# Performance work log

Measured on AMD Instinct MI355X. Metric: run time of the kernel, lower is better.

Reference implementation:

```python
import jax, jax.numpy as jnp
import numpy as np

NUM_CODES = 1024
CODE_DIM = 256
COMMIT_W = 0.25
EPS = 1e-5
ENT_LO, ENT_HI = 0.5, 0.9
ENT_W = 0.1
VAR_FLOOR = 0.05
VAR_W = 1e-3
DECORR_W = 1e-3


def setup_inputs() -> dict:
    key = jax.random.key(0)
    k1, k2, k3 = jax.random.split(key, 3)
    inputs = jax.random.normal(k1, (16, 2048, CODE_DIM), dtype=jnp.float32)
    weight = jax.random.normal(k2, (NUM_CODES, CODE_DIM), dtype=jnp.float32) * 0.1
    usage_counts = jax.random.uniform(k3, (NUM_CODES,), dtype=jnp.float32)
    return {"inputs": inputs, "weight": weight, "usage_counts": usage_counts}


def reference(inputs, weight, usage_counts):
    K, D = weight.shape
    flat = inputs.reshape(-1, D)  # [N, D]
    # squared euclidean distances [N, K]
    dist = (flat ** 2).sum(axis=1, keepdims=True) - 2.0 * flat @ weight.T + (weight ** 2).sum(axis=1)
    idx = jnp.argmin(dist, axis=1)  # [N]
    quant = weight[idx].reshape(inputs.shape)

    commitment_loss = COMMIT_W * jnp.mean((jax.lax.stop_gradient(quant) - inputs) ** 2)
    # straight-through estimator
    quant_ste = inputs + jax.lax.stop_gradient(quant - inputs)

    # usage entropy regularizer
    probs = usage_counts + EPS
    probs = probs / jnp.maximum(probs.sum(), EPS * K)
    usage_entropy = -jnp.sum(probs * jnp.log(probs + EPS)) / np.log(float(K)).astype(np.float32)
    gap = jnp.where(usage_entropy < ENT_LO, ENT_LO - usage_entropy,
                    jnp.where(usage_entropy > ENT_HI, usage_entropy - ENT_HI, 0.0))
    entropy_loss = ENT_W * gap ** 2

    # variance floor penalty on codebook
    variance = jnp.var(weight, axis=0)
    variance_loss = VAR_W * jnp.mean(jax.nn.relu(VAR_FLOOR - variance))

    # decorrelation penalty
    wc = weight - weight.mean(axis=0, keepdims=True)
    cov = wc.T @ wc / float(K)  # [D, D]
    off_diag = cov - jnp.diag(jnp.diag(cov))
    decorrelation_loss = DECORR_W * jnp.mean(off_diag ** 2)

    total_loss = commitment_loss + entropy_loss + variance_loss + decorrelation_loss
    indices = idx.reshape(inputs.shape[:-1])
    return (quant_ste, indices, total_loss, commitment_loss, entropy_loss,
            variance_loss, decorrelation_loss, usage_entropy)
```

## Files before the change

kernel.cpp:

```cpp
#include <hip/hip_runtime.h>
#include <math.h>

#define DIMS   256
#define KCODES 1024
#define NTOT   32768
#define TAU    4.0e-4f

typedef __bf16 bf16x8 __attribute__((ext_vector_type(8)));
typedef float  f32x4  __attribute__((ext_vector_type(4)));

#define WS_COMMIT   0
#define WS_FLAGCNT  1
#define WS_DECORR   2
#define WS_COLSUM   16
#define WS_COLSQ    272
#define WS_WSQ      1024
#define WS_XSQ      2048
#define WS_FLAGS    34816
#define WS_CAND1    67584
#define WS_CAND2    329728
#define WS_CANDI    591872
#define WS_WP       854016

#define OUT_Q    0
#define OUT_IDX  8388608
#define OUT_SCAL 8421376


__global__ __launch_bounds__(256) void prep_kernel(const float* __restrict__ X,
                                                   const float* __restrict__ W,
                                                   __bf16* __restrict__ Xp,
                                                   __bf16* __restrict__ Wp2,
                                                   float* ws) {
  int b = blockIdx.x;
  int tid = threadIdx.x;
  if (b < 1056) {
    bool isW = b >= 1024;
    const float* src = isW ? W : X;
    __bf16* dst = isW ? Wp2 : Xp;
    int sqoff = isW ? WS_WSQ : WS_XSQ;
    int bb = isW ? b - 1024 : b;
    int kt = tid >> 5, mtl = (tid >> 4) & 1, lc = tid & 15;
    int row = bb * 32 + mtl * 16 + lc;
    int bt = row >> 7, c = row & 127;
    int wv = c >> 6, t = (c >> 4) & 3;
    size_t hibase = ((((size_t)(bt * 8 + kt) * 2 + wv) * 4 + t) * 2) * 512;
    const float* s = src + (size_t)row * DIMS + kt * 32;
    float sq = 0.f;
    #pragma unroll
    for (int kq = 0; kq < 4; kq++) {
      float4 u = *(const float4*)(s + kq * 8);
      float4 v = *(const float4*)(s + kq * 8 + 4);
      float f[8] = {u.x, u.y, u.z, u.w, v.x, v.y, v.z, v.w};
      bf16x8 hi, lo;
      #pragma unroll
      for (int e = 0; e < 8; e++) {
        __bf16 h = (__bf16)f[e];
        hi[e] = h;
        lo[e] = (__bf16)(f[e] - (float)h);
        sq = fmaf(f[e], f[e], sq);
      }
      size_t off = (size_t)(kq * 16 + lc) * 8;
      *(bf16x8*)&dst[hibase + off] = hi;
      *(bf16x8*)&dst[hibase + 512 + off] = lo;
    }
    atomicAdd(&ws[sqoff + row], sq);
  } else if (b < 1064) {
    int d = tid;
    int r0 = (b - 1056) * 128;
    float s = 0.f, sq = 0.f;
    #pragma unroll 8
    for (int k = 0; k < 128; k++) {
      float v = W[(size_t)(r0 + k) * DIMS + d];
      s += v;
      sq = fmaf(v, v, sq);
    }
    atomicAdd(&ws[WS_COLSUM + d], s);
    atomicAdd(&ws[WS_COLSQ + d], sq);
  } else {
    __shared__ float wi_s[KCODES];
    __shared__ float red2[256];
    __shared__ float miB;
    __shared__ float red[4];
    int i0 = b - 1064;
    #pragma unroll
    for (int q = 0; q < 4; q++) {
      int row = q * 256 + tid;
      wi_s[row] = W[(size_t)row * DIMS + i0];
    }
    __syncthreads();
    float pm = 0.f;
    #pragma unroll
    for (int q = 0; q < 4; q++) pm += wi_s[tid * 4 + q];
    red2[tid] = pm;
    __syncthreads();
    if (tid == 0) {
      float s = 0.f;
      for (int k = 0; k < 256; k++) s += red2[k];
      miB = s * (1.0f / 1024.0f);
    }
    int j = tid;
    float a0 = 0.f, sj = 0.f;
    for (int k = 0; k < KCODES; k += 4) {
      #pragma unroll
      for (int u = 0; u < 4; u++) {
        float wj = W[(size_t)(k + u) * DIMS + j];
        a0 = fmaf(wi_s[k + u], wj, a0);
        sj += wj;
      }
    }
    __syncthreads();
    const float inv = 1.0f / 1024.0f;
    float mj = sj * inv;
    float v = 0.f;
    float c0 = a0 * inv - miB * mj;
    if (i0 != j) v = c0 * c0;
    #pragma unroll
    for (int m = 32; m >= 1; m >>= 1) v += __shfl_xor(v, m);
    if ((j & 63) == 0) red[j >> 6] = v;
    __syncthreads();
    if (j == 0) atomicAdd(&ws[WS_DECORR], (red[0] + red[1]) + (red[2] + red[3]));
  }
}

__global__ __launch_bounds__(256, 2) void pass1_kernel(const __bf16* __restrict__ Xp,
                                                       const __bf16* __restrict__ Wp2,
                                                       float* ws) {
  __shared__ float wsqs[128];
  __shared__ float d1L[256];
  __shared__ float d2L[256];
  __shared__ int   i1L[256];

  int tid = threadIdx.x;
  int lane = tid & 63, wave = tid >> 6;
  int wm = wave >> 1, wn = wave & 1;
  int quad = lane >> 4, col = lane & 15;
  int l = blockIdx.x;
  int bm = (l & 7) * 32 + ((l >> 3) & 31);
  int bn = l >> 8;
  int rowBase = bm * 128, cb = bn * 128;

  if (tid < 128) wsqs[tid] = ws[WS_WSQ + cb + tid];

  f32x4 acc[4][4];
  #pragma unroll
  for (int i = 0; i < 4; i++)
    #pragma unroll
    for (int j = 0; j < 4; j++) acc[i][j] = (f32x4){0.f, 0.f, 0.f, 0.f};

  const bf16x8* ab = (const bf16x8*)(Xp + (size_t)bm * 65536 + wm * 4096) + lane;
  const bf16x8* bb = (const bf16x8*)(Wp2 + (size_t)bn * 65536 + wn * 4096) + lane;

  bf16x8 Af[2][8], Bf[2][8];
  #pragma unroll
  for (int f = 0; f < 4; f++) {
    Af[0][f * 2] = ab[f * 128];
    Af[0][f * 2 + 1] = ab[f * 128 + 64];
    Bf[0][f * 2] = bb[f * 128];
    Bf[0][f * 2 + 1] = bb[f * 128 + 64];
  }
  #pragma unroll
  for (int kt = 0; kt < 8; kt++) {
    const int cur = kt & 1, nxt = cur ^ 1;
    if (kt < 7) {
      const bf16x8* an = ab + (kt + 1) * 1024;
      const bf16x8* bv = bb + (kt + 1) * 1024;
      #pragma unroll
      for (int f = 0; f < 4; f++) {
        Af[nxt][f * 2] = an[f * 128];
        Af[nxt][f * 2 + 1] = an[f * 128 + 64];
        Bf[nxt][f * 2] = bv[f * 128];
        Bf[nxt][f * 2 + 1] = bv[f * 128 + 64];
      }
    }
    #pragma unroll
    for (int nt = 0; nt < 4; nt++) {
      #pragma unroll
      for (int mt = 0; mt < 4; mt++) {
        acc[mt][nt] = __builtin_amdgcn_mfma_f32_16x16x32_bf16(Af[cur][mt * 2], Bf[cur][nt * 2], acc[mt][nt], 0, 0, 0);
        acc[mt][nt] = __builtin_amdgcn_mfma_f32_16x16x32_bf16(Af[cur][mt * 2], Bf[cur][nt * 2 + 1], acc[mt][nt], 0, 0, 0);
        acc[mt][nt] = __builtin_amdgcn_mfma_f32_16x16x32_bf16(Af[cur][mt * 2 + 1], Bf[cur][nt * 2], acc[mt][nt], 0, 0, 0);
      }
    }
  }
  __syncthreads();

  #pragma unroll
  for (int mt = 0; mt < 4; mt++) {
    #pragma unroll
    for (int r = 0; r < 4; r++) {
      float d1 = 3.0e38f, d2 = 3.0e38f;
      int i1 = 0;
      #pragma unroll
      for (int nt = 0; nt < 4; nt++) {
        int lc = wn * 64 + nt * 16 + col;
        float d = wsqs[lc] - 2.0f * acc[mt][nt][r];
        int g = cb + lc;
        if (d < d1) { d2 = d1; d1 = d; i1 = g; }
        else if (d < d2) d2 = d;
      }
      #pragma unroll
      for (int m = 1; m < 16; m <<= 1) {
        float od1 = __shfl_xor(d1, m);
        int oi1 = __shfl_xor(i1, m);
        float od2 = __shfl_xor(d2, m);
        if (od1 < d1 || (od1 == d1 && oi1 < i1)) {
          d2 = fminf(d1, fminf(d2, od2));
          d1 = od1; i1 = oi1;
        } else {
          d2 = fminf(od1, fminf(d2, od2));
        }
      }
      if (col == 0) {
        int lr = wm * 64 + mt * 16 + quad * 4 + r;
        d1L[lr * 2 + wn] = d1;
        d2L[lr * 2 + wn] = d2;
        i1L[lr * 2 + wn] = i1;
      }
    }
  }
  __syncthreads();
  if (tid < 128) {
    float a1 = d1L[tid * 2], a2 = d2L[tid * 2];
    int ai = i1L[tid * 2];
    float b1 = d1L[tid * 2 + 1], b2 = d2L[tid * 2 + 1];
    int bi = i1L[tid * 2 + 1];
    float m1, m2; int mi;
    if (b1 < a1 || (b1 == a1 && bi < ai)) { m1 = b1; mi = bi; m2 = fminf(a1, b2); }
    else { m1 = a1; mi = ai; m2 = fminf(b1, a2); }
    int o = bn * NTOT + rowBase + tid;
    ws[WS_CAND1 + o] = m1;
    ws[WS_CAND2 + o] = m2;
    ((int*)ws)[WS_CANDI + o] = mi;
  }
}

__global__ __launch_bounds__(256) void pass2_kernel(const float* __restrict__ W,
                                                    float* __restrict__ outQ,
                                                    float* __restrict__ outIdx, float* ws) {
  __shared__ float p1L[4][64];
  __shared__ float p2L[4][64];
  __shared__ int   piL[4][64];
  __shared__ int   idx_s[64];
  int tid = threadIdx.x;
  int r0 = blockIdx.x * 64;
  int grp = tid >> 6, rl = tid & 63;
  int row = r0 + rl;
  const float* c1 = ws + WS_CAND1;
  const float* c2 = ws + WS_CAND2;
  const int* ci = (const int*)ws + WS_CANDI;
  {
    int oa = (2 * grp) * NTOT + row;
    int ob = (2 * grp + 1) * NTOT + row;
    float a1 = c1[oa], a2 = c2[oa];
    int ai = ci[oa];
    float b1 = c1[ob], b2 = c2[ob];
    int bi = ci[ob];
    float m1, m2; int mi;
    if (b1 < a1 || (b1 == a1 && bi < ai)) { m1 = b1; mi = bi; m2 = fminf(a1, b2); }
    else { m1 = a1; mi = ai; m2 = fminf(a2, b1); }
    p1L[grp][rl] = m1;
    p2L[grp][rl] = m2;
    piL[grp][rl] = mi;
  }
  __syncthreads();
  if (tid < 64) {
    float m1 = p1L[0][tid], m2 = p2L[0][tid];
    int mi = piL[0][tid];
    #pragma unroll
    for (int w = 1; w < 4; w++) {
      float b1 = p1L[w][tid], b2 = p2L[w][tid];
      int bi = piL[w][tid];
      if (b1 < m1 || (b1 == m1 && bi < mi)) { m2 = fminf(m1, b2); m1 = b1; mi = bi; }
      else { m2 = fminf(m2, b1); }
    }
    int rw = r0 + tid;
    outIdx[rw] = (float)mi;
    idx_s[tid] = mi;
    int* wsI = (int*)ws;
    if (m2 - m1 < TAU) {
      int p = atomicAdd(&wsI[WS_FLAGCNT], 1);
      wsI[WS_FLAGS + p] = rw;
    }
    float partial = ws[WS_XSQ + rw] + m1;
    #pragma unroll
    for (int m = 32; m >= 1; m >>= 1) partial += __shfl_xor(partial, m);
    if (tid == 0) atomicAdd(&ws[WS_COMMIT], partial);
  }
  __syncthreads();
  int wave = tid >> 6, lane = tid & 63;
  #pragma unroll 4
  for (int i = 0; i < 16; i++) {
    int rr = wave * 16 + i;
    int ix = idx_s[rr];
    float4 v = ((const float4*)(W + (size_t)ix * DIMS))[lane];
    ((float4*)(outQ + (size_t)(r0 + rr) * DIMS))[lane] = v;
  }
}

__global__ __launch_bounds__(256) void refine_kernel(const float* __restrict__ X,
                                                     const float* __restrict__ W,
                                                     float* __restrict__ outQ,
                                                     float* __restrict__ outIdx, float* ws,
                                                     const float* __restrict__ U,
                                                     float* __restrict__ out) {
  __shared__ float xs[DIMS];
  __shared__ double dm[256];
  __shared__ int im[256];
  __shared__ int chosen;
  int tid = threadIdx.x;
  if (blockIdx.x == 512) {
    __shared__ float red[256];
    float s = 0.f;
    for (int e = tid; e < KCODES; e += 256) s += U[e] + 1e-5f;
    red[tid] = s;
    __syncthreads();
    for (int st = 128; st >= 1; st >>= 1) {
      if (tid < st) red[tid] += red[tid + st];
      __syncthreads();
    }
    float S = red[0];
    __syncthreads();
    float denom = fmaxf(S, 1e-5f * 1024.0f);
    float h = 0.f;
    for (int e = tid; e < KCODES; e += 256) {
      float p = (U[e] + 1e-5f) / denom;
      h += p * logf(p + 1e-5f);
    }
    red[tid] = h;
    __syncthreads();
    for (int st = 128; st >= 1; st >>= 1) {
      if (tid < st) red[tid] += red[tid + st];
      __syncthreads();
    }
    float H = -red[0] / 6.93147180559945f;
    __syncthreads();
    float m = ws[WS_COLSUM + tid] * (1.0f / 1024.0f);
    float var = ws[WS_COLSQ + tid] * (1.0f / 1024.0f) - m * m;
    float r = 0.05f - var;
    red[tid] = r > 0.f ? r : 0.f;
    __syncthreads();
    for (int st = 128; st >= 1; st >>= 1) {
      if (tid < st) red[tid] += red[tid + st];
      __syncthreads();
    }
    if (tid == 0) {
      float varloss = 1e-3f * (red[0] / 256.0f);
      float gap = H < 0.5f ? (0.5f - H) : (H > 0.9f ? (H - 0.9f) : 0.0f);
      float entloss = 0.1f * gap * gap;
      float commit = 0.25f * ws[WS_COMMIT] / 8388608.0f;
      float dec = 1e-3f * ws[WS_DECORR] / 65536.0f;
      float* sc = out + OUT_SCAL;
      sc[0] = commit + entloss + varloss + dec;
      sc[1] = commit;
      sc[2] = entloss;
      sc[3] = varloss;
      sc[4] = dec;
      sc[5] = H;
    }
    return;
  }
  const int* wsI = (const int*)ws;
  int cnt = wsI[WS_FLAGCNT];
  const int* list = wsI + WS_FLAGS;
  for (int f = blockIdx.x; f < cnt; f += 512) {
    int row = list[f];
    __syncthreads();
    if (tid < 64) ((float4*)xs)[tid] = ((const float4*)(X + (size_t)row * DIMS))[tid];
    __syncthreads();
    double bd = 1.0e300;
    int bi = 0;
    for (int jj = 0; jj < 4; jj++) {
      int c = tid + 256 * jj;
      double a0 = 0.0, a1 = 0.0, a2 = 0.0, a3 = 0.0;
      const float* wr = W + (size_t)c * DIMS;
      #pragma unroll 4
      for (int d4 = 0; d4 < 64; d4++) {
        float4 w = ((const float4*)wr)[d4];
        float4 x = ((const float4*)xs)[d4];
        double e0 = (double)x.x - (double)w.x;
        double e1 = (double)x.y - (double)w.y;
        double e2 = (double)x.z - (double)w.z;
        double e3 = (double)x.w - (double)w.w;
        a0 += e0 * e0; a1 += e1 * e1; a2 += e2 * e2; a3 += e3 * e3;
      }
      double s = (a0 + a1) + (a2 + a3);
      if (s < bd) { bd = s; bi = c; }
    }
    dm[tid] = bd; im[tid] = bi;
    __syncthreads();
    for (int st = 128; st >= 1; st >>= 1) {
      if (tid < st) {
        if (dm[tid + st] < dm[tid] || (dm[tid + st] == dm[tid] && im[tid + st] < im[tid])) {
          dm[tid] = dm[tid + st]; im[tid] = im[tid + st];
        }
      }
      __syncthreads();
    }
    if (tid == 0) { chosen = im[0]; outIdx[row] = (float)im[0]; }
    __syncthreads();
    int ix = chosen;
    if (tid < 64)
      ((float4*)(outQ + (size_t)row * DIMS))[tid] = ((const float4*)(W + (size_t)ix * DIMS))[tid];
  }
}

extern "C" void kernel_launch(void* const* d_in, const int* in_sizes, int n_in, void* d_out,
                              int out_size, void* d_ws, size_t ws_size, hipStream_t stream) {
  const float* X = (const float*)d_in[0];
  const float* W = (const float*)d_in[1];
  const float* U = (const float*)d_in[2];
  float* out = (float*)d_out;
  float* ws = (float*)d_ws;
  __bf16* Xp = (__bf16*)(out + OUT_Q);
  __bf16* Wp2 = (__bf16*)(ws + WS_WP);

  hipMemsetAsync(d_ws, 0, 139264, stream);
  prep_kernel<<<1320, 256, 0, stream>>>(X, W, Xp, Wp2, ws);
  pass1_kernel<<<2048, 256, 0, stream>>>(Xp, Wp2, ws);
  pass2_kernel<<<512, 256, 0, stream>>>(W, out + OUT_Q, out + OUT_IDX, ws);
  refine_kernel<<<513, 256, 0, stream>>>(X, W, out + OUT_Q, out + OUT_IDX, ws, U, out);
}
```

Before: 232.1 us.

## Drop atomics and the big workspace memset, fold column stats into decorr blocks, retile pass1

Per-row squared norms are now reduced inside each block through shared memory and stored directly, replacing per-thread atomic adds. Because those slots are now written rather than accumulated, the workspace memset shrinks to the three scalar accumulators. The separate column-sum and column-square blocks are removed: each decorrelation block already streams every column, so it also accumulates the sum of squares and writes the stats for its own column, leaving 8 fewer blocks. The pass1 block-index mapping is reordered so that consecutive blocks share codebook and input tiles in groups, aiming for better L2 reuse. The main risk is that any later reader that still assumes the rest of the old memset range is zeroed would silently get wrong results.

```diff
diff --git a/kernel.cpp b/kernel.cpp
--- a/kernel.cpp
+++ b/kernel.cpp
@@ -35,6 +35,7 @@
   int b = blockIdx.x;
   int tid = threadIdx.x;
   if (b < 1056) {
+    __shared__ float sqred[256];
     bool isW = b >= 1024;
     const float* src = isW ? W : X;
     __bf16* dst = isW ? Wp2 : Xp;
@@ -64,25 +65,20 @@
       *(bf16x8*)&dst[hibase + off] = hi;
       *(bf16x8*)&dst[hibase + 512 + off] = lo;
     }
-    atomicAdd(&ws[sqoff + row], sq);
-  } else if (b < 1064) {
-    int d = tid;
-    int r0 = (b - 1056) * 128;
-    float s = 0.f, sq = 0.f;
-    #pragma unroll 8
-    for (int k = 0; k < 128; k++) {
-      float v = W[(size_t)(r0 + k) * DIMS + d];
-      s += v;
-      sq = fmaf(v, v, sq);
-    }
-    atomicAdd(&ws[WS_COLSUM + d], s);
-    atomicAdd(&ws[WS_COLSQ + d], sq);
+    sqred[tid] = sq;
+    __syncthreads();
+    if (tid < 32) {
+      float s8 = 0.f;
+      #pragma unroll
+      for (int k = 0; k < 8; k++) s8 += sqred[k * 32 + tid];
+      ws[sqoff + bb * 32 + tid] = s8;
+    }
   } else {
     __shared__ float wi_s[KCODES];
     __shared__ float red2[256];
     __shared__ float miB;
     __shared__ float red[4];
-    int i0 = b - 1064;
+    int i0 = b - 1056;
     #pragma unroll
     for (int q = 0; q < 4; q++) {
       int row = q * 256 + tid;
@@ -100,14 +96,19 @@
       miB = s * (1.0f / 1024.0f);
     }
     int j = tid;
-    float a0 = 0.f, sj = 0.f;
+    float a0 = 0.f, sj = 0.f, sqj = 0.f;
     for (int k = 0; k < KCODES; k += 4) {
       #pragma unroll
       for (int u = 0; u < 4; u++) {
         float wj = W[(size_t)(k + u) * DIMS + j];
         a0 = fmaf(wi_s[k + u], wj, a0);
         sj += wj;
-      }
+        sqj = fmaf(wj, wj, sqj);
+      }
+    }
+    if (j == i0) {
+      ws[WS_COLSUM + i0] = sj;
+      ws[WS_COLSQ + i0] = sqj;
     }
     __syncthreads();
     const float inv = 1.0f / 1024.0f;
@@ -136,8 +137,10 @@
   int wm = wave >> 1, wn = wave & 1;
   int quad = lane >> 4, col = lane & 15;
   int l = blockIdx.x;
-  int bm = (l & 7) * 32 + ((l >> 3) & 31);
-  int bn = l >> 8;
+  int x = l & 7;
+  int j = l >> 3;
+  int bm = x * 32 + (j & 15) + (j >> 7) * 16;
+  int bn = (j >> 4) & 7;
   int rowBase = bm * 128, cb = bn * 128;
 
   if (tid < 128) wsqs[tid] = ws[WS_WSQ + cb + tid];
@@ -146,7 +149,7 @@
   #pragma unroll
   for (int i = 0; i < 4; i++)
     #pragma unroll
-    for (int j = 0; j < 4; j++) acc[i][j] = (f32x4){0.f, 0.f, 0.f, 0.f};
+    for (int jj = 0; jj < 4; jj++) acc[i][jj] = (f32x4){0.f, 0.f, 0.f, 0.f};
 
   const bf16x8* ab = (const bf16x8*)(Xp + (size_t)bm * 65536 + wm * 4096) + lane;
   const bf16x8* bb = (const bf16x8*)(Wp2 + (size_t)bn * 65536 + wn * 4096) + lane;
@@ -415,8 +418,8 @@
   __bf16* Xp = (__bf16*)(out + OUT_Q);
   __bf16* Wp2 = (__bf16*)(ws + WS_WP);
 
-  hipMemsetAsync(d_ws, 0, 139264, stream);
-  prep_kernel<<<1320, 256, 0, stream>>>(X, W, Xp, Wp2, ws);
+  hipMemsetAsync(d_ws, 0, 12, stream);
+  prep_kernel<<<1312, 256, 0, stream>>>(X, W, Xp, Wp2, ws);
   pass1_kernel<<<2048, 256, 0, stream>>>(Xp, Wp2, ws);
   pass2_kernel<<<512, 256, 0, stream>>>(W, out + OUT_Q, out + OUT_IDX, ws);
   refine_kernel<<<513, 256, 0, stream>>>(X, W, out + OUT_Q, out + OUT_IDX, ws, U, out);
```

New measurement: 229.2 us. About the same (-1.2%).
